# Kernel optimization log

Measured on AMD Instinct MI355X. Metric: run time of the kernel, lower is better.

Reference implementation:

```python
import jax, jax.numpy as jnp
import numpy as np

N_WIRES = 4
N_LAYERS = 2
BSZ = 4096


def setup_inputs() -> dict:
    key = jax.random.key(0)
    k1, k2, k3 = jax.random.split(key, 3)
    return {
        "x": jax.random.normal(k1, (BSZ, 784), dtype=jnp.float32),
        "params": jax.random.normal(k2, (N_LAYERS, N_WIRES), dtype=jnp.float32),
        "W": jax.random.normal(k3, (10, 784), dtype=jnp.float32) * 0.03,
        "b": jnp.zeros((10,), dtype=jnp.float32),
    }


def _rz(state, theta, w):
    # RZ(theta) = diag(exp(-i theta/2), exp(+i theta/2)) on wire w (axis w+1)
    ph = jnp.exp(jnp.array([-0.5j, 0.5j], dtype=jnp.complex64) * theta)
    shape = [1, 1, 1, 1, 1]
    shape[w + 1] = 2
    return state * ph.reshape(shape)


def _cx(state, cw, tw):
    # CNOT with control cw, target tw (tw > cw): flip target axis where control=1
    s0 = jnp.take(state, 0, axis=cw + 1)
    s1 = jnp.take(state, 1, axis=cw + 1)
    s1 = jnp.flip(s1, axis=tw)  # after removing control axis, target axis index = tw
    return jnp.stack([s0, s1], axis=cw + 1)


def quantum_block(patch, params):
    # patch: [N, 4] angles; returns [N, 4] PauliZ expectations
    half = 0.5 * patch
    # RY(theta)|0> = [cos(theta/2), sin(theta/2)]
    amps = jnp.stack([jnp.cos(half), jnp.sin(half)], axis=-1).astype(jnp.complex64)  # [N,4,2]
    state = jnp.einsum('na,nb,nc,nd->nabcd', amps[:, 0], amps[:, 1], amps[:, 2], amps[:, 3])
    for i in range(N_LAYERS):
        for w in range(N_WIRES):
            state = _rz(state, params[i, w], w)
        for w in range(N_WIRES - 1):
            state = _cx(state, w, w + 1)
    probs = state.real ** 2 + state.imag ** 2  # [N,2,2,2,2]
    z = jnp.array([1.0, -1.0], dtype=jnp.float32)
    exps = []
    for w in range(N_WIRES):
        shape = [1, 1, 1, 1, 1]
        shape[w + 1] = 2
        exps.append(jnp.sum(probs * z.reshape(shape), axis=(1, 2, 3, 4)))
    return jnp.stack(exps, axis=-1)  # [N,4]


def reference(x, params, W, b):
    B = x.shape[0]
    # extract 2x2 patches in row-major (r, c) order, each flattened row-major
    img = x.reshape(B, 14, 2, 14, 2).transpose(0, 1, 3, 2, 4).reshape(B * 196, 4)
    feats = quantum_block(img, params).reshape(B, 196 * 4)  # [B, 784]
    logits = feats @ W.T + b
    return jax.nn.log_softmax(logits, axis=-1)
```

## Files before the change

### kernel.cpp

```cpp
#include <hip/hip_runtime.h>
#include <math.h>


#define BSZ 4096

#define DPP_ADD(v, ctrl, rmask)                                              \
    v += __int_as_float(__builtin_amdgcn_update_dpp(                         \
        0, __float_as_int(v), (ctrl), (rmask), 0xf, true))

__global__ __launch_bounds__(256) void quanv_fused_v2(
    const float* __restrict__ x,
    const float* __restrict__ W,
    const float* __restrict__ bias,
    float* __restrict__ out)
{
    __shared__ float sW[10 * 784];

    {
        const float4* Wv = (const float4*)W;
        float4* sWv = (float4*)sW;
        #pragma unroll
        for (int i = 0; i < 8; ++i) {
            int idx = threadIdx.x + i * 256;
            if (idx < 1960) sWv[idx] = Wv[idx];
        }
    }
    __syncthreads();

    const int tid  = threadIdx.x;
    const int wave = tid >> 6;
    const int lane = tid & 63;
    const int h    = lane >> 5;
    const int kl   = lane & 31;
    const int row  = blockIdx.x * 8 + wave * 2 + h;

    const float* __restrict__ xr = x + row * 784;

    float acc[10];
    #pragma unroll
    for (int o = 0; o < 10; ++o) acc[o] = 0.f;

    #pragma unroll
    for (int t = 0; t < 7; ++t) {
        const int k = t * 32 + kl;
        if (t < 6 || kl < 4) {
            const int r = k / 14;
            const int c = k - r * 14;
            const int base = r * 56 + c * 2;
            const float2 a01 = *(const float2*)(xr + base);
            const float2 a23 = *(const float2*)(xr + base + 28);
            const float f0 = __cosf(a01.x);
            const float f1 = __cosf(a01.y);
            const float f2 = f0 * __cosf(a23.x);
            const float f3 = f1 * __cosf(a23.y);
            const float* wk = sW + k * 4;
            #pragma unroll
            for (int o = 0; o < 10; ++o) {
                const float4 w4 = *(const float4*)(wk + o * 784);
                acc[o] = fmaf(f0, w4.x, acc[o]);
                acc[o] = fmaf(f1, w4.y, acc[o]);
                acc[o] = fmaf(f2, w4.z, acc[o]);
                acc[o] = fmaf(f3, w4.w, acc[o]);
            }
        }
    }

    #pragma unroll
    for (int o = 0; o < 10; ++o) {
        float v = acc[o];
        DPP_ADD(v, 0x111, 0xf);
        DPP_ADD(v, 0x112, 0xf);
        DPP_ADD(v, 0x114, 0xf);
        DPP_ADD(v, 0x118, 0xf);
        DPP_ADD(v, 0x142, 0xa);
        acc[o] = v;
    }

    if (kl == 31) {
        float lg[10];
        float m = -1e30f;
        #pragma unroll
        for (int o = 0; o < 10; ++o) {
            lg[o] = acc[o] + bias[o];
            m = fmaxf(m, lg[o]);
        }
        float s = 0.f;
        #pragma unroll
        for (int o = 0; o < 10; ++o) s += __expf(lg[o] - m);
        const float lse = __logf(s) + m;
        float* orow = out + row * 10;
        #pragma unroll
        for (int o = 0; o < 10; ++o) orow[o] = lg[o] - lse;
    }
}

extern "C" void kernel_launch(void* const* d_in, const int* in_sizes, int n_in,
                              void* d_out, int out_size, void* d_ws, size_t ws_size,
                              hipStream_t stream) {
    const float* x    = (const float*)d_in[0];
    const float* W    = (const float*)d_in[2];
    const float* bias = (const float*)d_in[3];
    float* out = (float*)d_out;

    dim3 grid(BSZ / 8);
    dim3 block(256);
    quanv_fused_v2<<<grid, block, 0, stream>>>(x, W, bias, out);
}
```

Before: 9.977 us.

## Stage W via async global-to-LDS loads and overlap with x loads and cosines

Copies the weight matrix into shared memory with direct global-to-LDS load instructions, so the data no longer passes through registers. The x patch loads and cosine feature computation for all seven tiles are hoisted ahead of the barrier, so they overlap with the in-flight W transfer. The cost is higher register pressure from keeping all seven tiles' features live. Correctness depends on the barrier waiting for the LDS DMA to finish and on the per-lane LDS addressing of the builtin.

```diff
diff --git a/kernel.cpp b/kernel.cpp
--- a/kernel.cpp
+++ b/kernel.cpp
@@ -8,7 +8,13 @@
     v += __int_as_float(__builtin_amdgcn_update_dpp(                         \
         0, __float_as_int(v), (ctrl), (rmask), 0xf, true))
 
-__global__ __launch_bounds__(256) void quanv_fused_v2(
+__device__ __forceinline__ void load_lds16(const void* g, void* l) {
+    __builtin_amdgcn_global_load_lds(
+        (const __attribute__((address_space(1))) void*)g,
+        (__attribute__((address_space(3))) void*)l, 16, 0, 0);
+}
+
+__global__ __launch_bounds__(256) void quanv_fused_v3(
     const float* __restrict__ x,
     const float* __restrict__ W,
     const float* __restrict__ bias,
@@ -16,18 +22,18 @@
 {
     __shared__ float sW[10 * 784];
 
+    const int tid = threadIdx.x;
+
     {
         const float4* Wv = (const float4*)W;
         float4* sWv = (float4*)sW;
         #pragma unroll
         for (int i = 0; i < 8; ++i) {
-            int idx = threadIdx.x + i * 256;
-            if (idx < 1960) sWv[idx] = Wv[idx];
+            const int idx = tid + i * 256;
+            if (idx < 1960) load_lds16(Wv + idx, sWv + idx);
         }
     }
-    __syncthreads();
 
-    const int tid  = threadIdx.x;
     const int wave = tid >> 6;
     const int lane = tid & 63;
     const int h    = lane >> 5;
@@ -35,6 +41,29 @@
     const int row  = blockIdx.x * 8 + wave * 2 + h;
 
     const float* __restrict__ xr = x + row * 784;
+
+    float2 a01[7], a23[7];
+    #pragma unroll
+    for (int t = 0; t < 7; ++t) {
+        const int k = t * 32 + kl;
+        const int kk = (t < 6 || kl < 4) ? k : 0;
+        const int r = kk / 14;
+        const int c = kk - r * 14;
+        const int base = r * 56 + c * 2;
+        a01[t] = *(const float2*)(xr + base);
+        a23[t] = *(const float2*)(xr + base + 28);
+    }
+
+    float f[7][4];
+    #pragma unroll
+    for (int t = 0; t < 7; ++t) {
+        f[t][0] = __cosf(a01[t].x);
+        f[t][1] = __cosf(a01[t].y);
+        f[t][2] = f[t][0] * __cosf(a23[t].x);
+        f[t][3] = f[t][1] * __cosf(a23[t].y);
+    }
+
+    __syncthreads();
 
     float acc[10];
     #pragma unroll
@@ -44,23 +73,14 @@
     for (int t = 0; t < 7; ++t) {
         const int k = t * 32 + kl;
         if (t < 6 || kl < 4) {
-            const int r = k / 14;
-            const int c = k - r * 14;
-            const int base = r * 56 + c * 2;
-            const float2 a01 = *(const float2*)(xr + base);
-            const float2 a23 = *(const float2*)(xr + base + 28);
-            const float f0 = __cosf(a01.x);
-            const float f1 = __cosf(a01.y);
-            const float f2 = f0 * __cosf(a23.x);
-            const float f3 = f1 * __cosf(a23.y);
             const float* wk = sW + k * 4;
             #pragma unroll
             for (int o = 0; o < 10; ++o) {
                 const float4 w4 = *(const float4*)(wk + o * 784);
-                acc[o] = fmaf(f0, w4.x, acc[o]);
-                acc[o] = fmaf(f1, w4.y, acc[o]);
-                acc[o] = fmaf(f2, w4.z, acc[o]);
-                acc[o] = fmaf(f3, w4.w, acc[o]);
+                acc[o] = fmaf(f[t][0], w4.x, acc[o]);
+                acc[o] = fmaf(f[t][1], w4.y, acc[o]);
+                acc[o] = fmaf(f[t][2], w4.z, acc[o]);
+                acc[o] = fmaf(f[t][3], w4.w, acc[o]);
             }
         }
     }
@@ -104,5 +124,5 @@
 
     dim3 grid(BSZ / 8);
     dim3 block(256);
-    quanv_fused_v2<<<grid, block, 0, stream>>>(x, W, bias, out);
+    quanv_fused_v3<<<grid, block, 0, stream>>>(x, W, bias, out);
 }
```

Result: slower. 10.25 us (+2.7%).
